# Performance work log

Hardware: AMD Instinct MI355X
Metric: run time of the kernel (lower is better)

## Reference

```python
import jax, jax.numpy as jnp
import numpy as np

B, T, Fd, C, D = 16, 256, 128, 32, 32
K_RATIO = 0.5
EPS = 1e-5


def setup_inputs() -> dict:
    key = jax.random.key(0)
    ks = jax.random.split(key, 40)
    n = lambda i, shape, s=0.05: jax.random.normal(ks[i], shape, jnp.float32) * s
    inp = {"x": jax.random.normal(ks[0], (B, T, Fd, C), jnp.float32)}
    inp.update(c1w=n(1, (C, C)), c1b=n(2, (C,)), bng=1.0 + n(3, (C,)), bnb=n(4, (C,)),
               bnm=n(5, (C,)), bnv=jax.random.uniform(ks[6], (C,)) + 0.5,
               c2w=n(7, (1, C)), c2b=n(8, (1,)))
    def gat_params(i0, pre):
        return {pre + "apw": n(i0, (D, C)), pre + "apb": n(i0 + 1, (D,)),
                pre + "aw": n(i0 + 2, (D,)), pre + "pww": n(i0 + 3, (D, C)),
                pre + "pwb": n(i0 + 4, (D,)), pre + "pow": n(i0 + 5, (D, C)),
                pre + "pob": n(i0 + 6, (D,)), pre + "g": 1.0 + n(i0 + 7, (D,)),
                pre + "be": n(i0 + 8, (D,)), pre + "m": n(i0 + 9, (D,)),
                pre + "v": jax.random.uniform(ks[i0 + 10], (D,)) + 0.5}
    inp.update(gat_params(9, "fc_"))
    inp.update(gat_params(20, "tc_"))
    inp.update(pfw=n(31, (1, D)), pfb=n(32, (1,)), ptw=n(33, (1, D)), ptb=n(34, (1,)),
               w1=n(35, (D, D)), w2=n(36, (D, D)), fcw=n(37, (2, 2 * D)), fcb=n(38, (2,)))
    return inp


def _gat(h, apw, apb, aw, pww, pwb, poww, pob, g, be, mu, var):
    # h: (B, N, C). Dense pairwise multiplication -> (B, N, N, C)
    p = h[:, :, None, :] * h[:, None, :, :]
    e = jnp.tanh(jnp.einsum('bijc,dc->bijd', p, apw) + apb)      # (B,N,N,D)
    att = jax.nn.softmax(jnp.einsum('bijd,d->bij', e, aw), axis=2)  # softmax over dim=-2 (temp=1)
    out = jnp.einsum('bij,bjc->bic', att, h) @ pww.T + pwb + h @ poww.T + pob
    out = (out - mu) / jnp.sqrt(var + EPS) * g + be               # BatchNorm1d (eval)
    return jax.nn.selu(out)


def _pool(h, pw, pb, ratio):
    s = jax.nn.sigmoid(h @ pw.T + pb)                # (B,N,1)
    kn = max(int(h.shape[1] * ratio), 1)
    _, idx = jax.lax.top_k(s[..., 0], kn)            # (B,kn), descending scores
    return jnp.take_along_axis(h * s, idx[..., None], axis=1)


def reference(x, c1w, c1b, bng, bnb, bnm, bnv, c2w, c2b,
              fc_apw, fc_apb, fc_aw, fc_pww, fc_pwb, fc_pow, fc_pob, fc_g, fc_be, fc_m, fc_v,
              tc_apw, tc_apb, tc_aw, tc_pww, tc_pwb, tc_pow, tc_pob, tc_g, tc_be, tc_m, tc_v,
              pfw, pfb, ptw, ptb, w1, w2, fcw, fcb):
    # conv1 (1x1), SELU, BatchNorm2d (eval), conv2 (1x1 -> 1 channel)
    xp = jnp.einsum('oc,btfc->botf', c1w, x) + c1b[None, :, None, None]
    xp = jax.nn.selu(xp)
    xp = (xp - bnm[None, :, None, None]) / jnp.sqrt(bnv + EPS)[None, :, None, None] \
         * bng[None, :, None, None] + bnb[None, :, None, None]
    m = jnp.einsum('c,bctf->btf', c2w[0], xp) + c2b[0]           # (B,T,F)
    M0 = jax.nn.softmax(m, axis=1)
    FCatt = jnp.einsum('btf,btfc->bfc', M0, x)                   # sum over T
    TCatt = jnp.einsum('btf,btfc->btc', M0, x)                   # sum over F
    FC_gat = _gat(FCatt, fc_apw, fc_apb, fc_aw, fc_pww, fc_pwb, fc_pow, fc_pob, fc_g, fc_be, fc_m, fc_v)
    TC_gat = _gat(TCatt, tc_apw, tc_apb, tc_aw, tc_pww, tc_pwb, tc_pow, tc_pob, tc_g, tc_be, tc_m, tc_v)
    xF = _pool(FC_gat, pfw, pfb, K_RATIO)                        # (B, F/2, D)
    xT = _pool(TC_gat, ptw, ptb, K_RATIO)                        # (B, T/2, D)
    M1 = jax.nn.softmax((xF @ w1.T) @ xT.transpose(0, 2, 1), axis=-1)
    M2 = jax.nn.softmax((xT @ w2.T) @ xF.transpose(0, 2, 1), axis=-1)
    xF_fused = xF + M1 @ xT
    xT_fused = xT + M2 @ xF
    node = jnp.concatenate([xF_fused.max(axis=1), xT_fused.max(axis=1)], axis=-1)
    return node @ fcw.T + fcb
```

## Files before the change

### kernel.cpp

```cpp
#include <hip/hip_runtime.h>
#include <hip/hip_bf16.h>

#define Bn 16
#define Tn 256
#define Fn 128
#define Cn 32
#define Dn 32
#define EPSf 1e-5f
#define SELU_L 1.0507009873554805f
#define SELU_A 1.6732632423543772f

typedef unsigned short u16;
typedef unsigned int u32;

struct Ptrs { const void* p[39]; };

#define P_C1W 0
#define P_C1B 1024
#define P_MW  1056
#define P_MK  1088
#define P_FC  1089
#define P_TCG (1089+3264)
#define G_APW 0
#define G_APB 1024
#define G_AW  1056
#define G_PWW 1088
#define G_PWB 2112
#define G_POW 2144
#define G_POB 3168
#define G_GS  3200
#define G_GB  3232
#define GAT_SZ 3264
#define P_PFW (P_TCG+GAT_SZ)
#define P_PFB (P_PFW+32)
#define P_PTW (P_PFB+1)
#define P_PTB (P_PTW+32)
#define P_W1  (P_PTB+1)
#define P_W2  (P_W1+1024)
#define P_FCW (P_W2+1024)
#define P_FCB (P_FCW+128)
#define P_FLAG 10000

#define WS_M     10240
#define WS_FCATT (WS_M+524288)
#define WS_TCATT (WS_FCATT+65536)
#define WS_FCGAT (WS_TCATT+131072)
#define WS_TCGAT (WS_FCGAT+65536)
#define WS_XF    (WS_TCGAT+131072)
#define WS_XT    (WS_XF+32768)
#define WS_XFF   (WS_XT+65536)
#define WS_XTF   (WS_XFF+32768)

__device__ __forceinline__ float bf2f(u16 u) {
    union { u32 i; float f; } v; v.i = ((u32)u) << 16; return v.f;
}
__device__ __forceinline__ u16 f2bf(float f) {
    union { float f; u32 u; } v; v.f = f;
    u32 r = (v.u + 0x7fffu + ((v.u >> 16) & 1u)) >> 16;
    return (u16)r;
}
__device__ __forceinline__ void up2(u32 u, float* o) {
    union { u32 i; float f; } a, b;
    a.i = u << 16; b.i = u & 0xffff0000u;
    o[0] = a.f; o[1] = b.f;
}
__device__ __forceinline__ float tanh_fast(float x) {
    float e = __expf(2.f * x);
    return 1.f - 2.f / (e + 1.f);
}
__device__ __forceinline__ float ldp(const void* p, int i, int isb) {
    return isb ? bf2f(((const u16*)p)[i]) : ((const float*)p)[i];
}

__global__ __launch_bounds__(256) void k0_setup(Ptrs in, float* __restrict__ P) {
    __shared__ int sflag;
    int tid = threadIdx.x;
    int blk = blockIdx.x;
    if (tid < 64) {
        const u16* xu = (const u16*)in.p[0];
        int bad = 0;
        #pragma unroll
        for (int q = 0; q < 4; q++) {
            float f = bf2f(xu[tid * 4 + q]);
            float a = fabsf(f);
            if (!(a < 64.f) && !(a == 0.f)) bad++;
        }
        #pragma unroll
        for (int off = 32; off >= 1; off >>= 1) bad += __shfl_xor(bad, off, 64);
        if (tid == 0) sflag = (bad <= 8) ? 1 : 0;
    }
    __syncthreads();
    const int isb = sflag;

    if (blk == 0) {
        if (tid == 0) P[P_FLAG] = (float)isb;
        for (int i = tid; i < 1024; i += 256) P[P_C1W + i] = ldp(in.p[1], i, isb);
        if (tid < 32) {
            float A = ldp(in.p[3], tid, isb) * rsqrtf(ldp(in.p[6], tid, isb) + EPSf);
            float w = ldp(in.p[7], tid, isb);
            P[P_C1B + tid] = ldp(in.p[2], tid, isb);
            P[P_MW + tid] = w * A * SELU_L;
            float Bc = ldp(in.p[4], tid, isb) - ldp(in.p[5], tid, isb) * A;
            float term = w * Bc;
            #pragma unroll
            for (int off = 16; off >= 1; off >>= 1) term += __shfl_xor(term, off, 64);
            if (tid == 0) P[P_MK] = term + ldp(in.p[8], 0, isb);
        }
        if (tid >= 64 && tid < 96) {
            int t = tid - 64;
            P[P_PFW + t] = ldp(in.p[31], t, isb);
            P[P_PTW + t] = ldp(in.p[33], t, isb);
        }
        if (tid == 96) { P[P_PFB] = ldp(in.p[32], 0, isb); P[P_PTB] = ldp(in.p[34], 0, isb); }
        if (tid == 97) P[P_FCB]     = ldp(in.p[38], 0, isb);
        if (tid == 98) P[P_FCB + 1] = ldp(in.p[38], 1, isb);
        if (tid >= 128) P[P_FCW + (tid - 128)] = ldp(in.p[37], tid - 128, isb);
    } else if (blk <= 2) {
        int g = blk - 1;
        int ib = g ? 20 : 9;
        float* G = P + (g ? P_TCG : P_FC);
        for (int i = tid; i < 1024; i += 256) {
            G[G_APW + i] = ldp(in.p[ib + 0], i, isb);
            G[G_PWW + i] = ldp(in.p[ib + 3], i, isb);
            G[G_POW + i] = ldp(in.p[ib + 5], i, isb);
        }
        if (tid < 32) {
            G[G_APB + tid] = ldp(in.p[ib + 1], tid, isb);
            G[G_AW  + tid] = ldp(in.p[ib + 2], tid, isb);
            G[G_PWB + tid] = ldp(in.p[ib + 4], tid, isb);
            G[G_POB + tid] = ldp(in.p[ib + 6], tid, isb);
            float gs = ldp(in.p[ib + 7], tid, isb) * rsqrtf(ldp(in.p[ib + 10], tid, isb) + EPSf);
            G[G_GS + tid] = gs;
            G[G_GB + tid] = ldp(in.p[ib + 8], tid, isb) - ldp(in.p[ib + 9], tid, isb) * gs;
        }
    } else {
        for (int i = tid; i < 1024; i += 256) {
            P[P_W1 + i] = ldp(in.p[35], i, isb);
            P[P_W2 + i] = ldp(in.p[36], i, isb);
        }
    }
}

__global__ __launch_bounds__(256) void k1_conv_m(const void* __restrict__ xin,
                                                 const float* __restrict__ P,
                                                 float* __restrict__ M) {
    int idx = blockIdx.x * 256 + threadIdx.x;
    const int isb = __builtin_amdgcn_readfirstlane((int)P[P_FLAG]);
    float xv[32];
    if (isb) {
        const uint4* xp4 = reinterpret_cast<const uint4*>((const u16*)xin + (size_t)idx * 32);
        uint4 q0 = xp4[0], q1 = xp4[1], q2 = xp4[2], q3 = xp4[3];
        up2(q0.x, xv + 0);  up2(q0.y, xv + 2);  up2(q0.z, xv + 4);  up2(q0.w, xv + 6);
        up2(q1.x, xv + 8);  up2(q1.y, xv + 10); up2(q1.z, xv + 12); up2(q1.w, xv + 14);
        up2(q2.x, xv + 16); up2(q2.y, xv + 18); up2(q2.z, xv + 20); up2(q2.w, xv + 22);
        up2(q3.x, xv + 24); up2(q3.y, xv + 26); up2(q3.z, xv + 28); up2(q3.w, xv + 30);
    } else {
        const float4* xf4 = reinterpret_cast<const float4*>((const float*)xin + (size_t)idx * 32);
        #pragma unroll
        for (int q = 0; q < 8; q++) {
            float4 v = xf4[q];
            xv[q * 4 + 0] = v.x; xv[q * 4 + 1] = v.y;
            xv[q * 4 + 2] = v.z; xv[q * 4 + 3] = v.w;
        }
    }
    float acc = P[P_MK];
    #pragma unroll
    for (int o = 0; o < 32; o++) {
        float z = P[P_C1B + o];
        #pragma unroll
        for (int c = 0; c < 32; c++) z = fmaf(P[P_C1W + o * 32 + c], xv[c], z);
        float br = (z > 0.f) ? z : SELU_A * (__expf(z) - 1.f);
        acc = fmaf(P[P_MW + o], br, acc);
    }
    M[idx] = acc;
}

__global__ __launch_bounds__(256) void k2_softmax(float* __restrict__ M,
                                                  float* __restrict__ FCzero) {
    __shared__ float r[256];
    int b = blockIdx.x >> 3, fg = blockIdx.x & 7;
    int tid = threadIdx.x;
    int fl = tid & 15, ts = tid >> 4;
    float* col = M + (size_t)b * (Tn * Fn) + fg * 16 + fl;
    float v[16];
    float mx = -1e30f;
    #pragma unroll
    for (int k = 0; k < 16; k++) { v[k] = col[(ts * 16 + k) * Fn]; mx = fmaxf(mx, v[k]); }
    r[tid] = mx; __syncthreads();
    for (int s = 128; s >= 16; s >>= 1) { if (tid < s) r[tid] = fmaxf(r[tid], r[tid + s]); __syncthreads(); }
    mx = r[fl];
    __syncthreads();
    float sm = 0.f;
    #pragma unroll
    for (int k = 0; k < 16; k++) { v[k] = __expf(v[k] - mx); sm += v[k]; }
    r[tid] = sm; __syncthreads();
    for (int s = 128; s >= 16; s >>= 1) { if (tid < s) r[tid] += r[tid + s]; __syncthreads(); }
    float inv = 1.f / r[fl];
    #pragma unroll
    for (int k = 0; k < 16; k++) col[(ts * 16 + k) * Fn] = v[k] * inv;
    int gid = blockIdx.x * 256 + tid;
    for (int i = gid; i < Bn * Fn * Cn; i += 128 * 256) FCzero[i] = 0.f;
}

__global__ __launch_bounds__(256) void k3n(const void* __restrict__ xin,
                                           const float* __restrict__ M,
                                           const float* __restrict__ Pflag,
                                           float* __restrict__ FCatt,
                                           float* __restrict__ TCatt) {
    __shared__ float lA[256], lB[256];
    int bi = blockIdx.x;
    int b = bi >> 5, tg = bi & 31;
    int tid = threadIdx.x;
    const int isb = __builtin_amdgcn_readfirstlane((int)Pflag[P_FLAG]);
    float fa0[8], fa1[8];
    #pragma unroll
    for (int k = 0; k < 8; k++) { fa0[k] = 0.f; fa1[k] = 0.f; }
    int fbase = tid >> 4;
    for (int tt = 0; tt < 8; tt++) {
        int t = tg * 8 + tt;
        const float* Mrow = M + (size_t)b * (Tn * Fn) + (size_t)t * Fn;
        size_t rowoff = ((size_t)b * Tn + t) * (Fn * Cn);
        float ts0 = 0.f, ts1 = 0.f;
        #pragma unroll
        for (int k = 0; k < 8; k++) {
            float x0, x1;
            if (isb) {
                u32 u = *(const u32*)((const u16*)xin + rowoff + tid * 2 + 512 * k);
                float tmp[2]; up2(u, tmp); x0 = tmp[0]; x1 = tmp[1];
            } else {
                float2 v2 = *(const float2*)((const float*)xin + rowoff + tid * 2 + 512 * k);
                x0 = v2.x; x1 = v2.y;
            }
            float m = Mrow[fbase + 16 * k];
            x0 *= m; x1 *= m;
            fa0[k] += x0; fa1[k] += x1;
            ts0 += x0; ts1 += x1;
        }
        lA[tid] = ts0; lB[tid] = ts1;
        __syncthreads();
        if (tid < 32) {
            int half = tid & 1, p = tid >> 1;
            float s = 0.f;
            if (half) { for (int g = 0; g < 16; g++) s += lB[g * 16 + p]; }
            else      { for (int g = 0; g < 16; g++) s += lA[g * 16 + p]; }
            TCatt[((size_t)b * Tn + t) * Cn + tid] = s;
        }
        __syncthreads();
    }
    #pragma unroll
    for (int k = 0; k < 8; k++) {
        atomicAdd(&FCatt[(size_t)b * 4096 + tid * 2 + 512 * k],     fa0[k]);
        atomicAdd(&FCatt[(size_t)b * 4096 + tid * 2 + 512 * k + 1], fa1[k]);
    }
}

__global__ __launch_bounds__(256) void k4a_scores(const float* __restrict__ P,
                                                  const float* __restrict__ FCatt,
                                                  const float* __restrict__ TCatt,
                                                  u16* __restrict__ SFC,
                                                  u16* __restrict__ STC) {
    __shared__ float li[16 * 33], lj[16 * 33];
    int bi = blockIdx.x;
    int N, nt, b, pr; const float* h; u16* S; const float* G;
    if (bi < 16 * 36) { b = bi / 36; pr = bi % 36; N = 128; nt = 8;
        h = FCatt + (size_t)b * 4096; S = SFC + (size_t)b * 16384; G = P + P_FC; }
    else { bi -= 16 * 36; b = bi / 136; pr = bi % 136; N = 256; nt = 16;
        h = TCatt + (size_t)b * 8192; S = STC + (size_t)b * 65536; G = P + P_TCG; }
    int ti = 0, rem = pr;
    while (rem >= nt - ti) { rem -= nt - ti; ti++; }
    int tj = ti + rem;
    int tid = threadIdx.x;
    for (int e = tid; e < 512; e += 256) {
        int rr = e >> 5, c = e & 31;
        li[rr * 33 + c] = h[(ti * 16 + rr) * 32 + c];
        lj[rr * 33 + c] = h[(tj * 16 + rr) * 32 + c];
    }
    __syncthreads();
    int il = tid >> 4, jl = tid & 15;
    float p[32];
    #pragma unroll
    for (int c = 0; c < 32; c++) p[c] = li[il * 33 + c] * lj[jl * 33 + c];
    float score = 0.f;
    #pragma unroll
    for (int d = 0; d < 32; d++) {
        float z = G[G_APB + d];
        #pragma unroll
        for (int c = 0; c < 32; c++) z = fmaf(G[G_APW + d * 32 + c], p[c], z);
        score = fmaf(G[G_AW + d], tanh_fast(z), score);
    }
    int i = ti * 16 + il, j = tj * 16 + jl;
    u16 sb = f2bf(score);
    S[(size_t)i * N + j] = sb;
    if (ti != tj) S[(size_t)j * N + i] = sb;
}

__global__ __launch_bounds__(256) void k4b_soft(const float* __restrict__ P,
                                                const float* __restrict__ FCatt,
                                                const float* __restrict__ TCatt,
                                                const u16* __restrict__ SFC,
                                                const u16* __restrict__ STC,
                                                float* __restrict__ FCgat,
                                                float* __restrict__ TCgat) {
    __shared__ float hs[256 * 33];
    __shared__ float sc[256];
    __shared__ float red[256];
    __shared__ float wred[8];
    int bi = blockIdx.x;
    int N, b, i; const float* h; float* out; const float* G; const u16* Srow;
    if (bi < 2048) { N = 128; b = bi >> 7; i = bi & 127;
        h = FCatt + (size_t)b * 4096; out = FCgat + (size_t)b * 4096; G = P + P_FC;
        Srow = SFC + (size_t)b * 16384 + (size_t)i * 128; }
    else { bi -= 2048; N = 256; b = bi >> 8; i = bi & 255;
        h = TCatt + (size_t)b * 8192; out = TCgat + (size_t)b * 8192; G = P + P_TCG;
        Srow = STC + (size_t)b * 65536 + (size_t)i * 256; }
    int tid = threadIdx.x;
    int lane = tid & 63, w = tid >> 6;
    const float4* h4 = reinterpret_cast<const float4*>(h);
    for (int el = tid; el < N * 8; el += 256) {
        float4 v = h4[el];
        int j = el >> 3, c = (el & 7) * 4;
        float* dst = &hs[j * 33 + c];
        dst[0] = v.x; dst[1] = v.y; dst[2] = v.z; dst[3] = v.w;
    }
    float sv = (tid < N) ? bf2f(Srow[tid]) : -1e30f;
    float wm = sv;
    #pragma unroll
    for (int off = 32; off >= 1; off >>= 1) wm = fmaxf(wm, __shfl_xor(wm, off, 64));
    if (lane == 0) wred[w] = wm;
    __syncthreads();
    float mx = fmaxf(fmaxf(wred[0], wred[1]), fmaxf(wred[2], wred[3]));
    float e = (tid < N) ? __expf(sv - mx) : 0.f;
    sc[tid] = e;
    float wsum = e;
    #pragma unroll
    for (int off = 32; off >= 1; off >>= 1) wsum += __shfl_xor(wsum, off, 64);
    if (lane == 0) wred[4 + w] = wsum;
    __syncthreads();
    float inv = 1.f / (wred[4] + wred[5] + wred[6] + wred[7]);
    int jg = tid >> 5, c0 = tid & 31;
    float acc = 0.f;
    for (int j = jg; j < N; j += 8) acc = fmaf(sc[j], hs[j * 33 + c0], acc);
    red[tid] = acc;
    __syncthreads();
    if (tid < 32) {
        float asum = 0.f;
        #pragma unroll
        for (int g = 0; g < 8; g++) asum += red[tid + 32 * g];
        red[tid] = asum * inv;
        int d = tid;
        float z = G[G_PWB + d] + G[G_POB + d];
        #pragma unroll
        for (int c = 0; c < 32; c++)
            z = fmaf(G[G_PWW + d * 32 + c], red[c], fmaf(G[G_POW + d * 32 + c], hs[i * 33 + c], z));
        z = z * G[G_GS + d] + G[G_GB + d];
        z = SELU_L * ((z > 0.f) ? z : SELU_A * (__expf(z) - 1.f));
        out[(size_t)i * 32 + d] = z;
    }
}

__global__ __launch_bounds__(256) void k5_pool(const float* __restrict__ P,
                                               const float* __restrict__ FCgat,
                                               const float* __restrict__ TCgat,
                                               float* __restrict__ XF,
                                               float* __restrict__ XT) {
    __shared__ float s[256];
    int bi = blockIdx.x;
    int N, kn, b, pboff; const float* g; float* xp; const float* pw;
    if (bi < 16) { b = bi; N = 128; kn = 64;
        g = FCgat + (size_t)b * 4096; xp = XF + (size_t)b * 2048; pw = P + P_PFW; pboff = P_PFB; }
    else { b = bi - 16; N = 256; kn = 128;
        g = TCgat + (size_t)b * 8192; xp = XT + (size_t)b * 4096; pw = P + P_PTW; pboff = P_PTB; }
    int tid = threadIdx.x;
    float sv = 0.f;
    if (tid < N) {
        float z = P[pboff];
        #pragma unroll
        for (int d = 0; d < 32; d++) z = fmaf(pw[d], g[(size_t)tid * 32 + d], z);
        sv = 1.f / (1.f + __expf(-z));
        s[tid] = sv;
    }
    __syncthreads();
    if (tid < N) {
        int rank = 0;
        for (int l = 0; l < N; l++) {
            float sl = s[l];
            rank += (sl > sv) || (sl == sv && l < tid);
        }
        if (rank < kn) {
            #pragma unroll
            for (int d = 0; d < 32; d++) xp[(size_t)rank * 32 + d] = g[(size_t)tid * 32 + d] * sv;
        }
    }
}

__global__ __launch_bounds__(256) void k6_fuse(const float* __restrict__ P,
                                               const float* __restrict__ XF,
                                               const float* __restrict__ XT,
                                               float* __restrict__ XFF,
                                               float* __restrict__ XTF) {
    int wid = blockIdx.x * 4 + (threadIdx.x >> 6);
    int lane = threadIdx.x & 63;
    if (wid < 1024) {
        int b = wid >> 6, i = wid & 63;
        const float* xf  = XF + ((size_t)b * 64 + i) * 32;
        const float* xtb = XT + (size_t)b * 4096;
        const float* w1 = P + P_W1;
        int d = lane & 31;
        float y = 0.f;
        #pragma unroll
        for (int c = 0; c < 32; c++) y = fmaf(w1[d * 32 + c], xf[c], y);
        float xtr0[32], xtr1[32];
        #pragma unroll
        for (int c = 0; c < 32; c++) {
            xtr0[c] = xtb[(size_t)lane * 32 + c];
            xtr1[c] = xtb[(size_t)(lane + 64) * 32 + c];
        }
        float s0 = 0.f, s1 = 0.f;
        #pragma unroll
        for (int c = 0; c < 32; c++) {
            float yc = __shfl(y, c, 64);
            s0 = fmaf(yc, xtr0[c], s0);
            s1 = fmaf(yc, xtr1[c], s1);
        }
        float mx = fmaxf(s0, s1);
        #pragma unroll
        for (int off = 1; off < 64; off <<= 1) mx = fmaxf(mx, __shfl_xor(mx, off, 64));
        float e0 = __expf(s0 - mx), e1 = __expf(s1 - mx);
        float sm = e0 + e1;
        #pragma unroll
        for (int off = 1; off < 64; off <<= 1) sm += __shfl_xor(sm, off, 64);
        float inv = 1.f / sm;
        float a0 = e0 * inv, a1 = e1 * inv;
        float v[32];
        #pragma unroll
        for (int c = 0; c < 32; c++) v[c] = a0 * xtr0[c] + a1 * xtr1[c];
        #pragma unroll
        for (int off = 1; off < 64; off <<= 1) {
            #pragma unroll
            for (int c = 0; c < 32; c++) v[c] += __shfl_xor(v[c], off, 64);
        }
        if (lane == 0) {
            float* o = XFF + ((size_t)b * 64 + i) * 32;
            #pragma unroll
            for (int c = 0; c < 32; c++) o[c] = xf[c] + v[c];
        }
    } else {
        int r = wid - 1024;
        int b = r >> 7, i = r & 127;
        const float* xt  = XT + ((size_t)b * 128 + i) * 32;
        const float* xfb = XF + (size_t)b * 2048;
        const float* w2 = P + P_W2;
        int d = lane & 31;
        float y = 0.f;
        #pragma unroll
        for (int c = 0; c < 32; c++) y = fmaf(w2[d * 32 + c], xt[c], y);
        float xfr[32];
        #pragma unroll
        for (int c = 0; c < 32; c++) xfr[c] = xfb[(size_t)lane * 32 + c];
        float sc0 = 0.f;
        #pragma unroll
        for (int c = 0; c < 32; c++) sc0 = fmaf(__shfl(y, c, 64), xfr[c], sc0);
        float mx = sc0;
        #pragma unroll
        for (int off = 1; off < 64; off <<= 1) mx = fmaxf(mx, __shfl_xor(mx, off, 64));
        float e = __expf(sc0 - mx);
        float sm = e;
        #pragma unroll
        for (int off = 1; off < 64; off <<= 1) sm += __shfl_xor(sm, off, 64);
        float a = e / sm;
        float v[32];
        #pragma unroll
        for (int c = 0; c < 32; c++) v[c] = a * xfr[c];
        #pragma unroll
        for (int off = 1; off < 64; off <<= 1) {
            #pragma unroll
            for (int c = 0; c < 32; c++) v[c] += __shfl_xor(v[c], off, 64);
        }
        if (lane == 0) {
            float* o = XTF + ((size_t)b * 128 + i) * 32;
            #pragma unroll
            for (int c = 0; c < 32; c++) o[c] = xt[c] + v[c];
        }
    }
}

__global__ __launch_bounds__(64) void k7_out(const float* __restrict__ P,
                                             const float* __restrict__ XFF,
                                             const float* __restrict__ XTF,
                                             void* __restrict__ outp) {
    __shared__ float node[64];
    int b = blockIdx.x, tid = threadIdx.x;
    if (tid < 32) {
        float m = -1e30f;
        for (int r = 0; r < 64; r++) m = fmaxf(m, XFF[((size_t)b * 64 + r) * 32 + tid]);
        node[tid] = m;
    } else {
        int c = tid - 32;
        float m = -1e30f;
        for (int r = 0; r < 128; r++) m = fmaxf(m, XTF[((size_t)b * 128 + r) * 32 + c]);
        node[tid] = m;
    }
    __syncthreads();
    if (tid < 2) {
        float z = P[P_FCB + tid];
        #pragma unroll
        for (int k = 0; k < 64; k++) z = fmaf(P[P_FCW + tid * 64 + k], node[k], z);
        int isb = (int)P[P_FLAG];
        if (isb) ((u16*)outp)[b * 2 + tid] = f2bf(z);
        else     ((float*)outp)[b * 2 + tid] = z;
    }
}

extern "C" void kernel_launch(void* const* d_in, const int* in_sizes, int n_in,
                              void* d_out, int out_size, void* d_ws, size_t ws_size,
                              hipStream_t stream) {
    (void)in_sizes; (void)n_in; (void)out_size; (void)ws_size;
    float* W = (float*)d_ws;
    Ptrs ptrs;
    for (int i = 0; i < 39; i++) ptrs.p[i] = d_in[i];
    const void* x = d_in[0];
    float* P = W;
    u16* STC = (u16*)(W + WS_M);
    u16* SFC = (u16*)(W + WS_XF);

    k0_setup<<<4, 256, 0, stream>>>(ptrs, P);
    k1_conv_m<<<2048, 256, 0, stream>>>(x, P, W + WS_M);
    k2_softmax<<<128, 256, 0, stream>>>(W + WS_M, W + WS_FCATT);
    k3n<<<512, 256, 0, stream>>>(x, W + WS_M, P, W + WS_FCATT, W + WS_TCATT);
    k4a_scores<<<16 * 36 + 16 * 136, 256, 0, stream>>>(P, W + WS_FCATT, W + WS_TCATT, SFC, STC);
    k4b_soft<<<6144, 256, 0, stream>>>(P, W + WS_FCATT, W + WS_TCATT, SFC, STC,
                                       W + WS_FCGAT, W + WS_TCGAT);
    k5_pool<<<32, 256, 0, stream>>>(P, W + WS_FCGAT, W + WS_TCGAT, W + WS_XF, W + WS_XT);
    k6_fuse<<<768, 256, 0, stream>>>(P, W + WS_XF, W + WS_XT, W + WS_XFF, W + WS_XTF);
    k7_out<<<16, 64, 0, stream>>>(P, W + WS_XFF, W + WS_XTF, d_out);
}
```

Measured before the change: 324.0 us.

## Process 16 rows per block in GAT softmax and use shuffle reductions in k3n

The GAT softmax/aggregation kernel now handles 16 query rows per block, one row per wavefront per iteration. The h tile staged in shared memory is reused across all 16 rows instead of being reloaded for every row, and the block count drops from 6144 to 384. Reductions now use wavefront shuffles and per-wave score buffers instead of block-wide barriers. In k3n, the per-timestep TCatt reduction switches to shuffles plus a single barrier at the end instead of two barriers per timestep. The costs are fewer blocks to spread across the GPU and half of each wavefront's lanes computing duplicate work in the projection step.

```diff
diff --git a/kernel.cpp b/kernel.cpp
--- a/kernel.cpp
+++ b/kernel.cpp
@@ -207,10 +207,11 @@
                                            const float* __restrict__ Pflag,
                                            float* __restrict__ FCatt,
                                            float* __restrict__ TCatt) {
-    __shared__ float lA[256], lB[256];
+    __shared__ float part[4][8][32];
     int bi = blockIdx.x;
     int b = bi >> 5, tg = bi & 31;
     int tid = threadIdx.x;
+    int w = tid >> 6, lane = tid & 63;
     const int isb = __builtin_amdgcn_readfirstlane((int)Pflag[P_FLAG]);
     float fa0[8], fa1[8];
     #pragma unroll
@@ -236,16 +237,18 @@
             fa0[k] += x0; fa1[k] += x1;
             ts0 += x0; ts1 += x1;
         }
-        lA[tid] = ts0; lB[tid] = ts1;
-        __syncthreads();
-        if (tid < 32) {
-            int half = tid & 1, p = tid >> 1;
-            float s = 0.f;
-            if (half) { for (int g = 0; g < 16; g++) s += lB[g * 16 + p]; }
-            else      { for (int g = 0; g < 16; g++) s += lA[g * 16 + p]; }
-            TCatt[((size_t)b * Tn + t) * Cn + tid] = s;
-        }
-        __syncthreads();
+        ts0 += __shfl_xor(ts0, 16, 64); ts0 += __shfl_xor(ts0, 32, 64);
+        ts1 += __shfl_xor(ts1, 16, 64); ts1 += __shfl_xor(ts1, 32, 64);
+        if (lane < 16) {
+            part[w][tt][lane * 2]     = ts0;
+            part[w][tt][lane * 2 + 1] = ts1;
+        }
+    }
+    __syncthreads();
+    {
+        int tt = tid >> 5, c = tid & 31;
+        float s = part[0][tt][c] + part[1][tt][c] + part[2][tt][c] + part[3][tt][c];
+        TCatt[((size_t)b * Tn + tg * 8 + tt) * Cn + c] = s;
     }
     #pragma unroll
     for (int k = 0; k < 8; k++) {
@@ -301,60 +304,61 @@
                                                 const u16* __restrict__ STC,
                                                 float* __restrict__ FCgat,
                                                 float* __restrict__ TCgat) {
-    __shared__ float hs[256 * 33];
-    __shared__ float sc[256];
-    __shared__ float red[256];
-    __shared__ float wred[8];
+    __shared__ float hs[256 * 32];
+    __shared__ float scb[4][256];
     int bi = blockIdx.x;
-    int N, b, i; const float* h; float* out; const float* G; const u16* Srow;
-    if (bi < 2048) { N = 128; b = bi >> 7; i = bi & 127;
+    int N, b, rowbase; const float* h; float* out; const float* G; const u16* S;
+    if (bi < 128) {
+        N = 128; b = bi >> 3; rowbase = (bi & 7) * 16;
         h = FCatt + (size_t)b * 4096; out = FCgat + (size_t)b * 4096; G = P + P_FC;
-        Srow = SFC + (size_t)b * 16384 + (size_t)i * 128; }
-    else { bi -= 2048; N = 256; b = bi >> 8; i = bi & 255;
+        S = SFC + (size_t)b * 16384;
+    } else {
+        int t = bi - 128;
+        N = 256; b = t >> 4; rowbase = (t & 15) * 16;
         h = TCatt + (size_t)b * 8192; out = TCgat + (size_t)b * 8192; G = P + P_TCG;
-        Srow = STC + (size_t)b * 65536 + (size_t)i * 256; }
+        S = STC + (size_t)b * 65536;
+    }
     int tid = threadIdx.x;
-    int lane = tid & 63, w = tid >> 6;
+    int w = tid >> 6, lane = tid & 63;
     const float4* h4 = reinterpret_cast<const float4*>(h);
-    for (int el = tid; el < N * 8; el += 256) {
-        float4 v = h4[el];
-        int j = el >> 3, c = (el & 7) * 4;
-        float* dst = &hs[j * 33 + c];
-        dst[0] = v.x; dst[1] = v.y; dst[2] = v.z; dst[3] = v.w;
-    }
-    float sv = (tid < N) ? bf2f(Srow[tid]) : -1e30f;
-    float wm = sv;
-    #pragma unroll
-    for (int off = 32; off >= 1; off >>= 1) wm = fmaxf(wm, __shfl_xor(wm, off, 64));
-    if (lane == 0) wred[w] = wm;
-    __syncthreads();
-    float mx = fmaxf(fmaxf(wred[0], wred[1]), fmaxf(wred[2], wred[3]));
-    float e = (tid < N) ? __expf(sv - mx) : 0.f;
-    sc[tid] = e;
-    float wsum = e;
-    #pragma unroll
-    for (int off = 32; off >= 1; off >>= 1) wsum += __shfl_xor(wsum, off, 64);
-    if (lane == 0) wred[4 + w] = wsum;
-    __syncthreads();
-    float inv = 1.f / (wred[4] + wred[5] + wred[6] + wred[7]);
-    int jg = tid >> 5, c0 = tid & 31;
-    float acc = 0.f;
-    for (int j = jg; j < N; j += 8) acc = fmaf(sc[j], hs[j * 33 + c0], acc);
-    red[tid] = acc;
-    __syncthreads();
-    if (tid < 32) {
-        float asum = 0.f;
-        #pragma unroll
-        for (int g = 0; g < 8; g++) asum += red[tid + 32 * g];
-        red[tid] = asum * inv;
-        int d = tid;
+    float4* hs4 = reinterpret_cast<float4*>(hs);
+    for (int el = tid; el < N * 8; el += 256) hs4[el] = h4[el];
+    __syncthreads();
+
+    int c = lane & 31;
+    int nq = N >> 6;
+    for (int r = 0; r < 4; r++) {
+        int row = rowbase + w + 4 * r;
+        const u16* Srow = S + (size_t)row * N;
+        float v[4];
+        float mx = -1e30f;
+        for (int q = 0; q < nq; q++) { v[q] = bf2f(Srow[lane + 64 * q]); mx = fmaxf(mx, v[q]); }
+        #pragma unroll
+        for (int off = 32; off >= 1; off >>= 1) mx = fmaxf(mx, __shfl_xor(mx, off, 64));
+        float sum = 0.f;
+        for (int q = 0; q < nq; q++) {
+            float e = __expf(v[q] - mx);
+            scb[w][lane + 64 * q] = e;
+            sum += e;
+        }
+        #pragma unroll
+        for (int off = 32; off >= 1; off >>= 1) sum += __shfl_xor(sum, off, 64);
+        float inv = 1.f / sum;
+        asm volatile("s_waitcnt lgkmcnt(0)" ::: "memory");
+        int half = lane >> 5;
+        float acc = 0.f;
+        for (int j = half; j < N; j += 2) acc = fmaf(scb[w][j], hs[j * 32 + c], acc);
+        acc += __shfl_xor(acc, 32, 64);
+        acc *= inv;
+        int d = c;
         float z = G[G_PWB + d] + G[G_POB + d];
         #pragma unroll
-        for (int c = 0; c < 32; c++)
-            z = fmaf(G[G_PWW + d * 32 + c], red[c], fmaf(G[G_POW + d * 32 + c], hs[i * 33 + c], z));
+        for (int c2 = 0; c2 < 32; c2++)
+            z = fmaf(G[G_PWW + d * 32 + c2], __shfl(acc, c2, 64),
+                fmaf(G[G_POW + d * 32 + c2], hs[row * 32 + c2], z));
         z = z * G[G_GS + d] + G[G_GB + d];
         z = SELU_L * ((z > 0.f) ? z : SELU_A * (__expf(z) - 1.f));
-        out[(size_t)i * 32 + d] = z;
+        if (lane < 32) out[(size_t)row * 32 + d] = z;
     }
 }
 
@@ -528,8 +532,8 @@
     k2_softmax<<<128, 256, 0, stream>>>(W + WS_M, W + WS_FCATT);
     k3n<<<512, 256, 0, stream>>>(x, W + WS_M, P, W + WS_FCATT, W + WS_TCATT);
     k4a_scores<<<16 * 36 + 16 * 136, 256, 0, stream>>>(P, W + WS_FCATT, W + WS_TCATT, SFC, STC);
-    k4b_soft<<<6144, 256, 0, stream>>>(P, W + WS_FCATT, W + WS_TCATT, SFC, STC,
-                                       W + WS_FCGAT, W + WS_TCGAT);
+    k4b_soft<<<384, 256, 0, stream>>>(P, W + WS_FCATT, W + WS_TCATT, SFC, STC,
+                                      W + WS_FCGAT, W + WS_TCGAT);
     k5_pool<<<32, 256, 0, stream>>>(P, W + WS_FCGAT, W + WS_TCGAT, W + WS_XF, W + WS_XT);
     k6_fuse<<<768, 256, 0, stream>>>(P, W + WS_XF, W + WS_XT, W + WS_XFF, W + WS_XTF);
     k7_out<<<16, 64, 0, stream>>>(P, W + WS_XFF, W + WS_XTF, d_out);
```

Result: slower. 337.1 us (+4.0%).
